# Kernel optimization log

Measured on AMD Instinct MI355X. Metric: run time of the kernel, lower is better.

## Reference

```python
import jax, jax.numpy as jnp
import numpy as np

NUM_HEADS = 8
DIM = 512
B, S = 4, 2048
EPS = 1e-6


def _mha(x, wq, bq, wk, bk, wv, bv, wo, bo):
    # x: [B,S,D]; standard multi-head self-attention (tfa MultiHeadAttention math)
    Bx, Sx, D = x.shape
    hd = D // NUM_HEADS
    q = (x @ wq + bq).reshape(Bx, Sx, NUM_HEADS, hd)
    k = (x @ wk + bk).reshape(Bx, Sx, NUM_HEADS, hd)
    v = (x @ wv + bv).reshape(Bx, Sx, NUM_HEADS, hd)
    scores = jnp.einsum('bqhd,bkhd->bhqk', q, k) / jnp.sqrt(jnp.asarray(hd, x.dtype))
    attn = jax.nn.softmax(scores, axis=-1)
    out = jnp.einsum('bhqk,bkhd->bqhd', attn, v).reshape(Bx, Sx, D)
    return out @ wo + bo


def _ln(x, g, b):
    m = jnp.mean(x, axis=-1, keepdims=True)
    v = jnp.mean((x - m) ** 2, axis=-1, keepdims=True)
    return (x - m) * jax.lax.rsqrt(v + EPS) * g + b


def setup_inputs() -> dict:
    key = jax.random.key(0)
    ks = jax.random.split(key, 32)
    D, F = DIM, 4 * DIM
    std = 0.02
    def w(k, shape):
        return jax.random.normal(k, shape, dtype=jnp.float32) * std
    inp = {'x': jax.random.normal(ks[0], (B, S, D), dtype=jnp.float32)}
    # temporal attention params
    for i, nm in enumerate(['t', 's']):
        base = 1 + i * 8
        inp[nm + '_wq'] = w(ks[base + 0], (D, D)); inp[nm + '_bq'] = jnp.zeros((D,), jnp.float32)
        inp[nm + '_wk'] = w(ks[base + 1], (D, D)); inp[nm + '_bk'] = jnp.zeros((D,), jnp.float32)
        inp[nm + '_wv'] = w(ks[base + 2], (D, D)); inp[nm + '_bv'] = jnp.zeros((D,), jnp.float32)
        inp[nm + '_wo'] = w(ks[base + 3], (D, D)); inp[nm + '_bo'] = jnp.zeros((D,), jnp.float32)
    inp['ln1_g'] = jnp.ones((D,), jnp.float32); inp['ln1_b'] = jnp.zeros((D,), jnp.float32)
    inp['ln2_g'] = jnp.ones((D,), jnp.float32); inp['ln2_b'] = jnp.zeros((D,), jnp.float32)
    inp['f_w1'] = w(ks[20], (D, F)); inp['f_b1'] = jnp.zeros((F,), jnp.float32)
    inp['f_w2'] = w(ks[21], (F, D)); inp['f_b2'] = jnp.zeros((D,), jnp.float32)
    return inp


def reference(x,
              t_wq, t_bq, t_wk, t_bk, t_wv, t_bv, t_wo, t_bo,
              s_wq, s_bq, s_wk, s_bk, s_wv, s_bv, s_wo, s_bo,
              ln1_g, ln1_b, ln2_g, ln2_b,
              f_w1, f_b1, f_w2, f_b2):
    temporal = _mha(x, t_wq, t_bq, t_wk, t_bk, t_wv, t_bv, t_wo, t_bo)
    h = _ln(x + temporal, ln1_g, ln1_b)
    spatial = _mha(h, s_wq, s_bq, s_wk, s_bk, s_wv, s_bv, s_wo, s_bo)
    h2 = _ln(h + spatial, ln2_g, ln2_b)
    ffn = jax.nn.gelu(h2 @ f_w1 + f_b1, approximate=False) @ f_w2 + f_b2
    return h2 + ffn
```

## Files before the change

kernel.cpp:

```cpp
#include <hip/hip_runtime.h>

typedef __bf16 bf16x8 __attribute__((ext_vector_type(8)));
typedef float  f32x4  __attribute__((ext_vector_type(4)));

#define DEVI static __device__ __forceinline__

DEVI __bf16 tobf(float f) { return static_cast<__bf16>(f); }

__global__ __launch_bounds__(256) void cast_f32_bf16(
    const float* __restrict__ in, __bf16* __restrict__ out, int n8)
{
  int i = blockIdx.x * 256 + threadIdx.x;
  if (i >= n8) return;
  const float4* p = (const float4*)in + (size_t)i * 2;
  float4 a = p[0], b = p[1];
  bf16x8 o;
  o[0]=tobf(a.x); o[1]=tobf(a.y); o[2]=tobf(a.z); o[3]=tobf(a.w);
  o[4]=tobf(b.x); o[5]=tobf(b.y); o[6]=tobf(b.z); o[7]=tobf(b.w);
  ((bf16x8*)out)[i] = o;
}

__global__ __launch_bounds__(256) void transpose_cast(
    const float* __restrict__ W, __bf16* __restrict__ Wt, int R, int C)
{
  __shared__ float tile[32][33];
  const int tx = threadIdx.x & 31;
  const int ty = threadIdx.x >> 5;
  const int c0 = blockIdx.x * 32, r0 = blockIdx.y * 32;
  #pragma unroll
  for (int i = 0; i < 4; ++i)
    tile[ty + i*8][tx] = W[(size_t)(r0 + ty + i*8) * C + c0 + tx];
  __syncthreads();
  #pragma unroll
  for (int i = 0; i < 4; ++i)
    Wt[(size_t)(c0 + ty + i*8) * R + r0 + tx] = tobf(tile[tx][ty + i*8]);
}

__global__ __launch_bounds__(256) void concat3(
    const float* __restrict__ a, const float* __restrict__ b,
    const float* __restrict__ c, float* __restrict__ out, int n)
{
  int i = blockIdx.x * 256 + threadIdx.x;
  if (i < n) out[i] = a[i];
  else if (i < 2*n) out[i] = b[i - n];
  else if (i < 3*n) out[i] = c[i - 2*n];
}

__global__ __launch_bounds__(256)
void transpose_v(const __bf16* __restrict__ QKV, __bf16* __restrict__ VT)
{
  __shared__ __bf16 t[64][72];
  const int tid = threadIdx.x;
  const int bh = blockIdx.y;
  const int b = bh >> 3, h = bh & 7;
  const int s0 = blockIdx.x * 64;
  const int srow = tid >> 3, scol = (tid & 7) * 8;
  #pragma unroll
  for (int p = 0; p < 2; ++p) {
    const int row = srow + p * 32;
    *(bf16x8*)&t[row][scol] =
      *(const bf16x8*)(QKV + (size_t)(b * 2048 + s0 + row) * 1536 + 1024 + h * 64 + scol);
  }
  __syncthreads();
  #pragma unroll
  for (int p = 0; p < 2; ++p) {
    const int d = srow + p * 32;
    bf16x8 v;
    #pragma unroll
    for (int e = 0; e < 8; ++e) v[e] = t[scol + e][d];
    *(bf16x8*)(VT + ((size_t)bh * 64 + d) * 2048 + s0 + scol) = v;
  }
}

template<int EPI>
__global__ __launch_bounds__(256)
void gemm_bt(const __bf16* __restrict__ A, const __bf16* __restrict__ Bt,
             const float* __restrict__ bias, const float* __restrict__ resid,
             void* __restrict__ out, int M, int N, int K)
{
  __shared__ __bf16 As[128][72];
  __shared__ __bf16 Bs[128][72];
  const int tid  = threadIdx.x;
  const int lane = tid & 63;
  const int wave = tid >> 6;
  const int wm = wave >> 1, wn = wave & 1;
  const int m0 = blockIdx.x * 128, n0 = blockIdx.y * 128;
  const int lr = lane & 15, lg = lane >> 4;
  const int srow = tid >> 3, scol = (tid & 7) * 8;

  f32x4 acc[4][4];
  f32x4 zz = {0.f, 0.f, 0.f, 0.f};
  #pragma unroll
  for (int i = 0; i < 4; ++i)
    #pragma unroll
    for (int j = 0; j < 4; ++j) acc[i][j] = zz;

  for (int k0 = 0; k0 < K; k0 += 64) {
    #pragma unroll
    for (int p = 0; p < 4; ++p) {
      const int row = p * 32 + srow;
      *(bf16x8*)&As[row][scol] = *(const bf16x8*)(A  + (size_t)(m0 + row) * K + k0 + scol);
      *(bf16x8*)&Bs[row][scol] = *(const bf16x8*)(Bt + (size_t)(n0 + row) * K + k0 + scol);
    }
    __syncthreads();
    #pragma unroll
    for (int kk = 0; kk < 2; ++kk) {
      bf16x8 af[4], bfr[4];
      #pragma unroll
      for (int i = 0; i < 4; ++i) af[i]  = *(const bf16x8*)&As[wm*64 + i*16 + lr][kk*32 + lg*8];
      #pragma unroll
      for (int j = 0; j < 4; ++j) bfr[j] = *(const bf16x8*)&Bs[wn*64 + j*16 + lr][kk*32 + lg*8];
      #pragma unroll
      for (int i = 0; i < 4; ++i)
        #pragma unroll
        for (int j = 0; j < 4; ++j)
          acc[i][j] = __builtin_amdgcn_mfma_f32_16x16x32_bf16(af[i], bfr[j], acc[i][j], 0, 0, 0);
    }
    __syncthreads();
  }

  const int orow = m0 + wm * 64;
  const int ocol = n0 + wn * 64;
  #pragma unroll
  for (int j = 0; j < 4; ++j) {
    const int col = ocol + j*16 + lr;
    const float bv = bias[col];
    #pragma unroll
    for (int i = 0; i < 4; ++i) {
      #pragma unroll
      for (int r = 0; r < 4; ++r) {
        const int row = orow + i*16 + lg*4 + r;
        const size_t o = (size_t)row * N + col;
        float v = acc[i][j][r] + bv;
        if (EPI == 0) {
          ((__bf16*)out)[o] = tobf(v);
        } else if (EPI == 1) {
          float g = 0.5f * v * (1.0f + erff(v * 0.7071067811865476f));
          ((__bf16*)out)[o] = tobf(g);
        } else {
          ((float*)out)[o] = v + resid[o];
        }
      }
    }
  }
}

DEVI int sw_off(int row, int colByte) {
  return row * 128 + (colByte ^ ((row & 7) << 4));
}

__global__ __launch_bounds__(256)
void flash_attn(const __bf16* __restrict__ QKV, const __bf16* __restrict__ VT,
                __bf16* __restrict__ O)
{
  __shared__ __align__(16) char Ks [64 * 128];
  __shared__ __align__(16) char VTs[64 * 128];
  __shared__ __align__(16) char Ps [4 * 16 * 128];

  const int tid  = threadIdx.x;
  const int lane = tid & 63;
  const int w    = tid >> 6;
  const int lr = lane & 15, lg = lane >> 4;
  const int bh = blockIdx.y;
  const int b = bh >> 3, h = bh & 7;
  const int q0 = blockIdx.x * 64;
  const size_t qkvbase = (size_t)b * 2048 * 1536 + h * 64;
  const size_t vtbase  = (size_t)bh * 64 * 2048;
  const int srow = tid >> 3, scol = (tid & 7) * 8;

  bf16x8 aq[2];
  #pragma unroll
  for (int kk = 0; kk < 2; ++kk) {
    bf16x8 t = *(const bf16x8*)(QKV + qkvbase +
                 (size_t)(q0 + w*16 + lr) * 1536 + kk*32 + lg*8);
    #pragma unroll
    for (int e = 0; e < 8; ++e) t[e] = tobf(0.125f * (float)t[e]);
    aq[kk] = t;
  }

  float mrow[4], lrow[4];
  f32x4 oacc[4];
  f32x4 zz = {0.f, 0.f, 0.f, 0.f};
  #pragma unroll
  for (int r = 0; r < 4; ++r) { mrow[r] = -1e30f; lrow[r] = 0.f; }
  #pragma unroll
  for (int d = 0; d < 4; ++d) oacc[d] = zz;

  for (int kt = 0; kt < 32; ++kt) {
    const size_t kbase = qkvbase + 512 + (size_t)(kt * 64) * 1536;
    #pragma unroll
    for (int p = 0; p < 2; ++p) {
      const int row = srow + p * 32;
      *(bf16x8*)(Ks  + sw_off(row, scol * 2)) =
        *(const bf16x8*)(QKV + kbase + (size_t)row * 1536 + scol);
      *(bf16x8*)(VTs + sw_off(row, scol * 2)) =
        *(const bf16x8*)(VT + vtbase + (size_t)row * 2048 + kt * 64 + scol);
    }
    __syncthreads();

    f32x4 sf[4];
    __builtin_amdgcn_s_setprio(1);
    #pragma unroll
    for (int ct = 0; ct < 4; ++ct) {
      f32x4 s = zz;
      #pragma unroll
      for (int kk = 0; kk < 2; ++kk) {
        bf16x8 bb = *(const bf16x8*)(Ks + sw_off(ct*16 + lr, kk*64 + lg*16));
        s = __builtin_amdgcn_mfma_f32_16x16x32_bf16(aq[kk], bb, s, 0, 0, 0);
      }
      sf[ct] = s;
    }
    __builtin_amdgcn_s_setprio(0);

    #pragma unroll
    for (int r = 0; r < 4; ++r) {
      float tmax = fmaxf(fmaxf(sf[0][r], sf[1][r]), fmaxf(sf[2][r], sf[3][r]));
      #pragma unroll
      for (int off = 1; off < 16; off <<= 1) tmax = fmaxf(tmax, __shfl_xor(tmax, off));
      const float mnew = fmaxf(mrow[r], tmax);
      const float sc = __expf(mrow[r] - mnew);
      float psum = 0.f;
      #pragma unroll
      for (int ct = 0; ct < 4; ++ct) {
        float pv = __expf(sf[ct][r] - mnew);
        sf[ct][r] = pv;
        psum += pv;
      }
      #pragma unroll
      for (int off = 1; off < 16; off <<= 1) psum += __shfl_xor(psum, off);
      lrow[r] = lrow[r] * sc + psum;
      mrow[r] = mnew;
      #pragma unroll
      for (int d = 0; d < 4; ++d) oacc[d][r] *= sc;
    }

    #pragma unroll
    for (int ct = 0; ct < 4; ++ct)
      #pragma unroll
      for (int r = 0; r < 4; ++r)
        *(__bf16*)(Ps + w*2048 + sw_off(lg*4 + r, (ct*16 + lr) * 2)) = tobf(sf[ct][r]);

    __builtin_amdgcn_s_setprio(1);
    #pragma unroll
    for (int dt = 0; dt < 4; ++dt) {
      #pragma unroll
      for (int kk = 0; kk < 2; ++kk) {
        bf16x8 a  = *(const bf16x8*)(Ps  + w*2048 + sw_off(lr, kk*64 + lg*16));
        bf16x8 bb = *(const bf16x8*)(VTs + sw_off(dt*16 + lr, kk*64 + lg*16));
        oacc[dt] = __builtin_amdgcn_mfma_f32_16x16x32_bf16(a, bb, oacc[dt], 0, 0, 0);
      }
    }
    __builtin_amdgcn_s_setprio(0);
    __syncthreads();
  }

  float linv[4];
  #pragma unroll
  for (int r = 0; r < 4; ++r) linv[r] = 1.0f / lrow[r];
  #pragma unroll
  for (int dt = 0; dt < 4; ++dt)
    #pragma unroll
    for (int r = 0; r < 4; ++r) {
      const int row = q0 + w*16 + lg*4 + r;
      O[(size_t)(b * 2048 + row) * 512 + h*64 + dt*16 + lr] = tobf(oacc[dt][r] * linv[r]);
    }
}

__global__ __launch_bounds__(256)
void ln_kernel(const float* __restrict__ in, const float* __restrict__ gw,
               const float* __restrict__ bw, float* __restrict__ outF,
               __bf16* __restrict__ outB)
{
  const int lane = threadIdx.x & 63;
  const size_t row = (size_t)blockIdx.x * 4 + (threadIdx.x >> 6);
  const float* p = in + row * 512 + lane * 8;
  float4 v0 = *(const float4*)p;
  float4 v1 = *(const float4*)(p + 4);
  float s = (v0.x + v0.y) + (v0.z + v0.w) + (v1.x + v1.y) + (v1.z + v1.w);
  float q = v0.x*v0.x + v0.y*v0.y + v0.z*v0.z + v0.w*v0.w
          + v1.x*v1.x + v1.y*v1.y + v1.z*v1.z + v1.w*v1.w;
  #pragma unroll
  for (int off = 1; off < 64; off <<= 1) { s += __shfl_xor(s, off); q += __shfl_xor(q, off); }
  const float mean = s * (1.0f / 512.0f);
  const float var  = q * (1.0f / 512.0f) - mean * mean;
  const float rs   = rsqrtf(var + 1e-6f);
  const float4 g0 = *(const float4*)(gw + lane * 8);
  const float4 g1 = *(const float4*)(gw + lane * 8 + 4);
  const float4 b0 = *(const float4*)(bw + lane * 8);
  const float4 b1 = *(const float4*)(bw + lane * 8 + 4);
  float4 o0, o1;
  o0.x = (v0.x - mean) * rs * g0.x + b0.x;
  o0.y = (v0.y - mean) * rs * g0.y + b0.y;
  o0.z = (v0.z - mean) * rs * g0.z + b0.z;
  o0.w = (v0.w - mean) * rs * g0.w + b0.w;
  o1.x = (v1.x - mean) * rs * g1.x + b1.x;
  o1.y = (v1.y - mean) * rs * g1.y + b1.y;
  o1.z = (v1.z - mean) * rs * g1.z + b1.z;
  o1.w = (v1.w - mean) * rs * g1.w + b1.w;
  *(float4*)(outF + row * 512 + lane * 8)     = o0;
  *(float4*)(outF + row * 512 + lane * 8 + 4) = o1;
  bf16x8 ob;
  ob[0]=tobf(o0.x); ob[1]=tobf(o0.y); ob[2]=tobf(o0.z); ob[3]=tobf(o0.w);
  ob[4]=tobf(o1.x); ob[5]=tobf(o1.y); ob[6]=tobf(o1.z); ob[7]=tobf(o1.w);
  *(bf16x8*)(outB + row * 512 + lane * 8) = ob;
}

extern "C" void kernel_launch(void* const* d_in, const int* in_sizes, int n_in,
                              void* d_out, int out_size, void* d_ws, size_t ws_size,
                              hipStream_t stream)
{
  const float* x     = (const float*)d_in[0];
  const float* t_wq  = (const float*)d_in[1];
  const float* t_bq  = (const float*)d_in[2];
  const float* t_wk  = (const float*)d_in[3];
  const float* t_bk  = (const float*)d_in[4];
  const float* t_wv  = (const float*)d_in[5];
  const float* t_bv  = (const float*)d_in[6];
  const float* t_wo  = (const float*)d_in[7];
  const float* t_bo  = (const float*)d_in[8];
  const float* s_wq  = (const float*)d_in[9];
  const float* s_bq  = (const float*)d_in[10];
  const float* s_wk  = (const float*)d_in[11];
  const float* s_bk  = (const float*)d_in[12];
  const float* s_wv  = (const float*)d_in[13];
  const float* s_bv  = (const float*)d_in[14];
  const float* s_wo  = (const float*)d_in[15];
  const float* s_bo  = (const float*)d_in[16];
  const float* ln1_g = (const float*)d_in[17];
  const float* ln1_b = (const float*)d_in[18];
  const float* ln2_g = (const float*)d_in[19];
  const float* ln2_b = (const float*)d_in[20];
  const float* f_w1  = (const float*)d_in[21];
  const float* f_b1  = (const float*)d_in[22];
  const float* f_w2  = (const float*)d_in[23];
  const float* f_b2  = (const float*)d_in[24];

  char* ws = (char*)d_ws;
  size_t off = 0;
  auto alloc = [&](size_t bytes) -> void* {
    void* p = ws + off; off += (bytes + 255) & ~(size_t)255; return p;
  };

  __bf16* qkvb  = (__bf16*)alloc(8192ull * 1536 * 2);
  __bf16* attnb = (__bf16*)alloc(8192ull * 512 * 2);
  __bf16* gelu_b = qkvb;
  __bf16* xb    = (__bf16*)alloc(8192ull * 512 * 2);
  __bf16* h_bf  = xb;
  __bf16* vtb   = (__bf16*)alloc(8192ull * 512 * 2);
  __bf16* wT_t  = (__bf16*)alloc(1536ull * 512 * 2);
  __bf16* wT_s  = (__bf16*)alloc(1536ull * 512 * 2);
  __bf16* woT_t = (__bf16*)alloc(512ull * 512 * 2);
  __bf16* woT_s = (__bf16*)alloc(512ull * 512 * 2);
  __bf16* w1T   = (__bf16*)alloc(2048ull * 512 * 2);
  __bf16* w2T   = (__bf16*)alloc(512ull * 2048 * 2);
  float* bcat_t = (float*)alloc(1536 * 4);
  float* bcat_s = (float*)alloc(1536 * 4);
  float* tmp_f  = (float*)alloc(8192ull * 512 * 4);
  float* h_f    = (float*)alloc(8192ull * 512 * 4);
  float* h2_f   = (float*)alloc(8192ull * 512 * 4);
  __bf16* h2_bf = (__bf16*)alloc(8192ull * 512 * 2);
  (void)in_sizes; (void)n_in; (void)out_size; (void)ws_size;

  cast_f32_bf16<<<2048, 256, 0, stream>>>(x, xb, 524288);
  transpose_cast<<<dim3(16,16), 256, 0, stream>>>(t_wq, wT_t,               512, 512);
  transpose_cast<<<dim3(16,16), 256, 0, stream>>>(t_wk, wT_t + 512*512,     512, 512);
  transpose_cast<<<dim3(16,16), 256, 0, stream>>>(t_wv, wT_t + 2*512*512,   512, 512);
  transpose_cast<<<dim3(16,16), 256, 0, stream>>>(s_wq, wT_s,               512, 512);
  transpose_cast<<<dim3(16,16), 256, 0, stream>>>(s_wk, wT_s + 512*512,     512, 512);
  transpose_cast<<<dim3(16,16), 256, 0, stream>>>(s_wv, wT_s + 2*512*512,   512, 512);
  transpose_cast<<<dim3(16,16), 256, 0, stream>>>(t_wo, woT_t,              512, 512);
  transpose_cast<<<dim3(16,16), 256, 0, stream>>>(s_wo, woT_s,              512, 512);
  transpose_cast<<<dim3(64,16), 256, 0, stream>>>(f_w1, w1T,                512, 2048);
  transpose_cast<<<dim3(16,64), 256, 0, stream>>>(f_w2, w2T,                2048, 512);
  concat3<<<6, 256, 0, stream>>>(t_bq, t_bk, t_bv, bcat_t, 512);
  concat3<<<6, 256, 0, stream>>>(s_bq, s_bk, s_bv, bcat_s, 512);

  gemm_bt<0><<<dim3(64,12), 256, 0, stream>>>(xb, wT_t, bcat_t, nullptr, qkvb, 8192, 1536, 512);
  transpose_v<<<dim3(32,32), 256, 0, stream>>>(qkvb, vtb);
  flash_attn<<<dim3(32,32), 256, 0, stream>>>(qkvb, vtb, attnb);
  gemm_bt<2><<<dim3(64,4),  256, 0, stream>>>(attnb, woT_t, t_bo, x, tmp_f, 8192, 512, 512);
  ln_kernel<<<2048, 256, 0, stream>>>(tmp_f, ln1_g, ln1_b, h_f, h_bf);

  gemm_bt<0><<<dim3(64,12), 256, 0, stream>>>(h_bf, wT_s, bcat_s, nullptr, qkvb, 8192, 1536, 512);
  transpose_v<<<dim3(32,32), 256, 0, stream>>>(qkvb, vtb);
  flash_attn<<<dim3(32,32), 256, 0, stream>>>(qkvb, vtb, attnb);
  gemm_bt<2><<<dim3(64,4),  256, 0, stream>>>(attnb, woT_s, s_bo, h_f, tmp_f, 8192, 512, 512);
  ln_kernel<<<2048, 256, 0, stream>>>(tmp_f, ln2_g, ln2_b, h2_f, h2_bf);

  gemm_bt<1><<<dim3(64,16), 256, 0, stream>>>(h2_bf, w1T, f_b1, nullptr, gelu_b, 8192, 2048, 512);
  gemm_bt<2><<<dim3(64,4),  256, 0, stream>>>(gelu_b, w2T, f_b2, h2_f, (float*)d_out, 8192, 512, 2048);
}
```

Measured before the change: 534.9 us.

## Compute transposed scores in flash attention and pass P via register shuffles

Swaps the MFMA operands of the QK^T product so each lane holds the scores of a single query row. The softmax row max and sum then reduce within the lane plus two cross-lane shuffles, replacing the four-step shuffle reduction done for each of four rows. The probability tile is no longer written to and read back from shared memory; it is packed to bf16 and rearranged into the A-operand layout with lane shuffles. In exchange, the rescale factors and the final normalizer need extra broadcast shuffles, and correctness depends on the shuffle index mapping matching the MFMA layout.

Result: faster. 489.0 us (-8.6%).

```diff
diff --git a/kernel.cpp b/kernel.cpp
--- a/kernel.cpp
+++ b/kernel.cpp
@@ -6,6 +6,12 @@
 #define DEVI static __device__ __forceinline__
 
 DEVI __bf16 tobf(float f) { return static_cast<__bf16>(f); }
+
+DEVI unsigned pack2bf(float a, float b) {
+  union { __bf16 h[2]; unsigned u; } c;
+  c.h[0] = tobf(a); c.h[1] = tobf(b);
+  return c.u;
+}
 
 __global__ __launch_bounds__(256) void cast_f32_bf16(
     const float* __restrict__ in, __bf16* __restrict__ out, int n8)
@@ -155,7 +161,6 @@
 {
   __shared__ __align__(16) char Ks [64 * 128];
   __shared__ __align__(16) char VTs[64 * 128];
-  __shared__ __align__(16) char Ps [4 * 16 * 128];
 
   const int tid  = threadIdx.x;
   const int lane = tid & 63;
@@ -178,13 +183,15 @@
     aq[kk] = t;
   }
 
-  float mrow[4], lrow[4];
+  float mrow = -1e30f, lrow = 0.f;
   f32x4 oacc[4];
   f32x4 zz = {0.f, 0.f, 0.f, 0.f};
   #pragma unroll
-  for (int r = 0; r < 4; ++r) { mrow[r] = -1e30f; lrow[r] = 0.f; }
-  #pragma unroll
   for (int d = 0; d < 4; ++d) oacc[d] = zz;
+
+  const int srcA = lr + ((lg & 1) << 5);
+  const int srcB = srcA + 16;
+  const bool sel = ((lg >> 1) & 1) != 0;
 
   for (int kt = 0; kt < 32; ++kt) {
     const size_t kbase = qkvbase + 512 + (size_t)(kt * 64) * 1536;
@@ -205,49 +212,74 @@
       f32x4 s = zz;
       #pragma unroll
       for (int kk = 0; kk < 2; ++kk) {
-        bf16x8 bb = *(const bf16x8*)(Ks + sw_off(ct*16 + lr, kk*64 + lg*16));
-        s = __builtin_amdgcn_mfma_f32_16x16x32_bf16(aq[kk], bb, s, 0, 0, 0);
+        bf16x8 kf = *(const bf16x8*)(Ks + sw_off(ct*16 + lr, kk*64 + lg*16));
+        s = __builtin_amdgcn_mfma_f32_16x16x32_bf16(kf, aq[kk], s, 0, 0, 0);
       }
       sf[ct] = s;
     }
     __builtin_amdgcn_s_setprio(0);
 
-    #pragma unroll
-    for (int r = 0; r < 4; ++r) {
-      float tmax = fmaxf(fmaxf(sf[0][r], sf[1][r]), fmaxf(sf[2][r], sf[3][r]));
-      #pragma unroll
-      for (int off = 1; off < 16; off <<= 1) tmax = fmaxf(tmax, __shfl_xor(tmax, off));
-      const float mnew = fmaxf(mrow[r], tmax);
-      const float sc = __expf(mrow[r] - mnew);
-      float psum = 0.f;
-      #pragma unroll
-      for (int ct = 0; ct < 4; ++ct) {
+    float tmax = sf[0][0];
+    #pragma unroll
+    for (int ct = 0; ct < 4; ++ct)
+      #pragma unroll
+      for (int r = 0; r < 4; ++r) tmax = fmaxf(tmax, sf[ct][r]);
+    tmax = fmaxf(tmax, __shfl_xor(tmax, 16));
+    tmax = fmaxf(tmax, __shfl_xor(tmax, 32));
+    const float mnew = fmaxf(mrow, tmax);
+    const float sc = __expf(mrow - mnew);
+    float psum = 0.f;
+    #pragma unroll
+    for (int ct = 0; ct < 4; ++ct)
+      #pragma unroll
+      for (int r = 0; r < 4; ++r) {
         float pv = __expf(sf[ct][r] - mnew);
         sf[ct][r] = pv;
         psum += pv;
       }
-      #pragma unroll
-      for (int off = 1; off < 16; off <<= 1) psum += __shfl_xor(psum, off);
-      lrow[r] = lrow[r] * sc + psum;
-      mrow[r] = mnew;
-      #pragma unroll
-      for (int d = 0; d < 4; ++d) oacc[d][r] *= sc;
-    }
-
-    #pragma unroll
-    for (int ct = 0; ct < 4; ++ct)
-      #pragma unroll
-      for (int r = 0; r < 4; ++r)
-        *(__bf16*)(Ps + w*2048 + sw_off(lg*4 + r, (ct*16 + lr) * 2)) = tobf(sf[ct][r]);
+    psum += __shfl_xor(psum, 16);
+    psum += __shfl_xor(psum, 32);
+    lrow = lrow * sc + psum;
+    mrow = mnew;
+
+    float scq[4];
+    #pragma unroll
+    for (int r = 0; r < 4; ++r) scq[r] = __shfl(sc, lg*4 + r);
+    #pragma unroll
+    for (int dt = 0; dt < 4; ++dt)
+      #pragma unroll
+      for (int r = 0; r < 4; ++r) oacc[dt][r] *= scq[r];
+
+    unsigned pk0[4], pk1[4];
+    #pragma unroll
+    for (int ct = 0; ct < 4; ++ct) {
+      pk0[ct] = pack2bf(sf[ct][0], sf[ct][1]);
+      pk1[ct] = pack2bf(sf[ct][2], sf[ct][3]);
+    }
+
+    bf16x8 pa[2];
+    #pragma unroll
+    for (int kk = 0; kk < 2; ++kk) {
+      const int c0 = kk*2, c1 = kk*2 + 1;
+      unsigned a0 = __shfl(pk0[c0], srcA), a1 = __shfl(pk1[c0], srcA);
+      unsigned a2 = __shfl(pk0[c0], srcB), a3 = __shfl(pk1[c0], srcB);
+      unsigned b0 = __shfl(pk0[c1], srcA), b1 = __shfl(pk1[c1], srcA);
+      unsigned b2 = __shfl(pk0[c1], srcB), b3 = __shfl(pk1[c1], srcB);
+      union { unsigned u[4]; bf16x8 v; } cu;
+      cu.u[0] = sel ? b0 : a0;
+      cu.u[1] = sel ? b1 : a1;
+      cu.u[2] = sel ? b2 : a2;
+      cu.u[3] = sel ? b3 : a3;
+      pa[kk] = cu.v;
+    }
 
     __builtin_amdgcn_s_setprio(1);
     #pragma unroll
     for (int dt = 0; dt < 4; ++dt) {
       #pragma unroll
       for (int kk = 0; kk < 2; ++kk) {
-        bf16x8 a  = *(const bf16x8*)(Ps  + w*2048 + sw_off(lr, kk*64 + lg*16));
         bf16x8 bb = *(const bf16x8*)(VTs + sw_off(dt*16 + lr, kk*64 + lg*16));
-        oacc[dt] = __builtin_amdgcn_mfma_f32_16x16x32_bf16(a, bb, oacc[dt], 0, 0, 0);
+        oacc[dt] = __builtin_amdgcn_mfma_f32_16x16x32_bf16(pa[kk], bb, oacc[dt], 0, 0, 0);
       }
     }
     __builtin_amdgcn_s_setprio(0);
@@ -256,7 +288,10 @@
 
   float linv[4];
   #pragma unroll
-  for (int r = 0; r < 4; ++r) linv[r] = 1.0f / lrow[r];
+  for (int r = 0; r < 4; ++r) {
+    float lq = __shfl(lrow, lg*4 + r);
+    linv[r] = 1.0f / lq;
+  }
   #pragma unroll
   for (int dt = 0; dt < 4; ++dt)
     #pragma unroll
```
